# Kernel optimization log

Hardware: AMD Instinct MI355X
Metric: run time of the kernel (lower is better)

Reference implementation:

```python
import jax, jax.numpy as jnp
import numpy as np

B = 512      # batch
T = 16       # tokens per instruction
V = 1000     # vocab
E = 4        # num_experts
K = 1        # active experts per layer
NLAYERS = 3
TOPK_LOGIC = 32


def _conv(x, w, b, stride=2):
    # x: [B,Cin,H,W], w: [Cout,Cin,3,3] (OIHW), padding=1, stride=2
    y = jax.lax.conv_general_dilated(
        x, w, window_strides=(stride, stride), padding=((1, 1), (1, 1)),
        dimension_numbers=('NCHW', 'OIHW', 'NCHW'))
    return y + b[None, :, None, None]


def _gated_conv(x, w, b, gate):
    # w: [E,Cout,Cin,3,3], b: [E,Cout], gate: [B,E] 0/1 mask
    # Faithful to original: all experts computed densely, then masked.
    outs = jax.vmap(lambda wi, bi: _conv(x, wi, bi))(w, b)  # [E,B,Cout,H',W']
    return jnp.einsum('ebchw,be->bchw', outs, gate)


def _topk_mask(logits, k):
    # 0/1 mask with ones at the top-k positions along the last axis
    _, idx = jax.lax.top_k(logits, k)
    return jnp.sum(jax.nn.one_hot(idx, logits.shape[-1], dtype=logits.dtype), axis=-2)


def setup_inputs() -> dict:
    key = jax.random.key(0)
    ks = jax.random.split(key, 16)
    def rn(k, shape, s=0.05):
        return jax.random.normal(k, shape, jnp.float32) * s
    return dict(
        img=jax.random.normal(ks[0], (B, 12, 56, 56), jnp.float32),
        text=jax.random.randint(ks[1], (B, T), 0, V),
        prev_action=jax.random.randint(ks[2], (B,), 0, 7),
        emb_table=rn(ks[3], (V, 32), 1.0),
        r_w1=rn(ks[4], (32, 64)), r_b1=jnp.zeros((64,), jnp.float32),
        r_w2=rn(ks[5], (64, NLAYERS * E)), r_b2=jnp.zeros((NLAYERS * E,), jnp.float32),
        l_w1=rn(ks[6], (32, 64)), l_b1=jnp.zeros((64,), jnp.float32),
        l_w2=rn(ks[7], (64, 256)), l_b2=jnp.zeros((256,), jnp.float32),
        c1_w=rn(ks[8], (E, 32, 12, 3, 3)), c1_b=jnp.zeros((E, 32), jnp.float32),
        c2_w=rn(ks[9], (E, 64, 32, 3, 3)), c2_b=jnp.zeros((E, 64), jnp.float32),
        c3_w=rn(ks[10], (E, 128, 64, 3, 3)), c3_b=jnp.zeros((E, 128), jnp.float32),
        act_emb=rn(ks[11], (7, 16), 1.0),
        f_w=rn(ks[12], (6272 + 32 + 16, 256)), f_b=jnp.zeros((256,), jnp.float32),
        h_w=rn(ks[13], (256, 5)), h_b=jnp.zeros((5,), jnp.float32),
    )


def reference(img, text, prev_action, emb_table, r_w1, r_b1, r_w2, r_b2,
              l_w1, l_b1, l_w2, l_b2, c1_w, c1_b, c2_w, c2_b, c3_w, c3_b,
              act_emb, f_w, f_b, h_w, h_b):
    # EmbeddingBag(mode='mean') over token dim
    lang = jnp.mean(emb_table[text], axis=1)                      # [B,32]
    # Router: MLP -> [B,3,E] logits, top-k scatter -> 0/1 mask
    rlog = (jax.nn.relu(lang @ r_w1 + r_b1) @ r_w2 + r_b2).reshape(-1, NLAYERS, E)
    masks = _topk_mask(rlog, K)                                   # [B,3,E]
    x = jax.nn.relu(_gated_conv(img, c1_w, c1_b, masks[:, 0, :])) # [B,32,28,28]
    x = jax.nn.relu(_gated_conv(x, c2_w, c2_b, masks[:, 1, :]))   # [B,64,14,14]
    x = jax.nn.relu(_gated_conv(x, c3_w, c3_b, masks[:, 2, :]))   # [B,128,7,7]
    vis = x.reshape(x.shape[0], -1)                               # [B,6272]
    act = act_emb[prev_action]                                    # [B,16]
    fused = jnp.concatenate([vis, lang, act], axis=1)             # [B,6320]
    hidden = fused @ f_w + f_b                                    # [B,256]
    logic = jax.nn.relu(lang @ l_w1 + l_b1) @ l_w2 + l_b2         # [B,256]
    lmask = _topk_mask(logic, TOPK_LOGIC)                         # [B,256]
    out = jax.nn.relu(hidden * lmask)                             # dropout is identity in eval
    logits = out @ h_w + h_b                                      # [B,5]
    return logits, rlog
```

## Files before the change

kernel.cpp:

```cpp
#include <hip/hip_runtime.h>
#include <hip/hip_bf16.h>


typedef __bf16 bf16x8 __attribute__((ext_vector_type(8)));
typedef float f32x4 __attribute__((ext_vector_type(4)));
typedef unsigned short u16x8 __attribute__((ext_vector_type(8)));

__device__ __forceinline__ unsigned short f2bf(float f) {
  union { float f; unsigned u; } v; v.f = f;
  unsigned r = v.u + 0x7FFFu + ((v.u >> 16) & 1u);
  return (unsigned short)(r >> 16);
}

__global__ __launch_bounds__(256) void prep_kernel(
    const int* __restrict__ text, const float* __restrict__ emb,
    const float* __restrict__ r_w1, const float* __restrict__ r_b1,
    const float* __restrict__ r_w2, const float* __restrict__ r_b2,
    const float* __restrict__ l_w1, const float* __restrict__ l_b1,
    const float* __restrict__ l_w2, const float* __restrict__ l_b2,
    const float* __restrict__ act_emb, const int* __restrict__ pa,
    const float* __restrict__ c1_w, const float* __restrict__ c2_w,
    const float* __restrict__ c3_w, const float* __restrict__ fw,
    float* __restrict__ rlog_out, int* __restrict__ eidx, float* __restrict__ lmask,
    unsigned short* __restrict__ tailb,
    unsigned short* __restrict__ wb1, unsigned short* __restrict__ wb2,
    unsigned short* __restrict__ wb3, unsigned short* __restrict__ fwT) {
  __shared__ __align__(16) char shm[64 * 72 * 2];
  const int blk = blockIdx.x;
  const int tid = threadIdx.x;

  if (blk < 512) {
    int b = blk;
    int t = tid;
    __shared__ float lg[32];
    __shared__ float hr[64];
    __shared__ float hl[64];
    __shared__ float rl[12];
    __shared__ float lgc[256];

    if (t < 32) {
      const int* tb = text + b * 16;
      float s = 0.f;
#pragma unroll
      for (int tok = 0; tok < 16; ++tok) s += emb[tb[tok] * 32 + t];
      lg[t] = s * 0.0625f;
    }
    __syncthreads();

    if (t < 64) {
      float s1 = r_b1[t], s2 = l_b1[t];
      for (int k = 0; k < 32; ++k) {
        float lv = lg[k];
        s1 += lv * r_w1[k * 64 + t];
        s2 += lv * l_w1[k * 64 + t];
      }
      hr[t] = fmaxf(s1, 0.f);
      hl[t] = fmaxf(s2, 0.f);
    }
    if (t < 64) {
      float v = 0.f;
      if (t < 32) v = lg[t];
      else if (t < 48) v = act_emb[pa[b] * 16 + (t - 32)];
      tailb[b * 64 + t] = f2bf(v);
    }
    __syncthreads();

    if (t < 12) {
      float s = r_b2[t];
      for (int k = 0; k < 64; ++k) s += hr[k] * r_w2[k * 12 + t];
      rl[t] = s;
      rlog_out[b * 12 + t] = s;
    }
    {
      float s = l_b2[t];
      for (int k = 0; k < 64; ++k) s += hl[k] * l_w2[k * 256 + t];
      lgc[t] = s;
    }
    __syncthreads();

    if (t < 3) {
      int best = 0;
      float bv = rl[t * 4];
      for (int e = 1; e < 4; ++e) {
        float v = rl[t * 4 + e];
        if (v > bv) { bv = v; best = e; }
      }
      eidx[b * 3 + t] = best;
    }
    {
      float v = lgc[t];
      int cnt = 0;
      for (int k = 0; k < 256; ++k) {
        float u = lgc[k];
        cnt += (u > v) || (u == v && k < t);
      }
      lmask[b * 256 + t] = (cnt < 32) ? 1.f : 0.f;
    }
  } else if (blk < 2080) {
    int idx = (blk - 512) * 256 + tid;
    if (idx < 24576) {
      int k = idx % 192, ec = idx / 192;
      float v = 0.f;
      if (k < 144) {
        int g = k >> 4, ci = k & 15;
        if (ci < 12) v = c1_w[ec * 108 + ci * 9 + g];
      }
      wb1[idx] = f2bf(v);
    } else if (idx < 106496) {
      int i2 = idx - 24576;
      int k = i2 % 320, ec = i2 / 320;
      float v = 0.f;
      if (k < 288) {
        int g = k >> 5, ci = k & 31;
        v = c2_w[ec * 288 + ci * 9 + g];
      }
      wb2[i2] = f2bf(v);
    } else {
      int i3 = idx - 106496;
      int k = i3 % 576, ec = i3 / 576;
      int g = k >> 6, ci = k & 63;
      wb3[i3] = f2bf(c3_w[ec * 576 + ci * 9 + g]);
    }
  } else {
    unsigned short(*tl)[72] = (unsigned short(*)[72])shm;
    int fb = blk - 2080;
    int kblk = fb >> 2, nblk = fb & 3;
    int n0 = nblk * 64;
    int k0 = kblk * 64;
    int rl = tid >> 2;
    int c4 = (tid & 3) * 16;
    int srow;
    bool valid;
    if (kblk < 98) {
      int p = kblk >> 1;
      int c0 = (kblk & 1) * 64;
      srow = (c0 + rl) * 49 + p;
      valid = true;
    } else {
      srow = 6272 + rl;
      valid = (rl < 48);
    }
#pragma unroll
    for (int h = 0; h < 4; ++h) {
      float4 v = valid ? *(const float4*)&fw[(size_t)srow * 256 + n0 + c4 + h * 4]
                       : (float4){0.f, 0.f, 0.f, 0.f};
      tl[rl][c4 + h * 4 + 0] = f2bf(v.x);
      tl[rl][c4 + h * 4 + 1] = f2bf(v.y);
      tl[rl][c4 + h * 4 + 2] = f2bf(v.z);
      tl[rl][c4 + h * 4 + 3] = f2bf(v.w);
    }
    __syncthreads();
    int nloc = tid >> 2;
    int kc = (tid & 3) * 16;
    unsigned short vv[16];
#pragma unroll
    for (int i = 0; i < 16; ++i) vv[i] = tl[kc + i][nloc];
    unsigned short* dst = fwT + (size_t)(n0 + nloc) * 6336 + k0 + kc;
    *(uint4*)dst = *(const uint4*)&vv[0];
    *(uint4*)(dst + 8) = *(const uint4*)&vv[8];
  }
}

__global__ __launch_bounds__(256) void bucket_kernel(const int* __restrict__ eidx,
                                                     int* __restrict__ cnt,
                                                     int* __restrict__ perm) {
  int l = blockIdx.x;
  __shared__ int el[512];
  __shared__ int cc[4];
  int t = threadIdx.x;
  el[t] = eidx[t * 3 + l];
  el[t + 256] = eidx[(t + 256) * 3 + l];
  __syncthreads();
  if (t < 4) {
    int c = 0;
    for (int b = 0; b < 512; ++b) c += (el[b] == t);
    cc[t] = c;
    cnt[l * 4 + t] = c;
  }
  __syncthreads();
#pragma unroll
  for (int rep = 0; rep < 2; ++rep) {
    int b = t + rep * 256;
    int e = el[b];
    int rank = 0;
    for (int bp = 0; bp < b; ++bp) rank += (el[bp] == e);
    int off = 0;
    for (int ee = 0; ee < e; ++ee) off += cc[ee];
    perm[l * 512 + off + rank] = b;
  }
}

__global__ __launch_bounds__(256) void conv1_fused(
    const float* __restrict__ img, const unsigned short* __restrict__ wb,
    const float* __restrict__ bias, const int* __restrict__ eidx,
    unsigned short* __restrict__ out) {
  const int s = blockIdx.x / 7;
  const int t = blockIdx.x % 7;
  const int e = eidx[s * 3];
  __shared__ __align__(16) unsigned short lds_in[12288];
  __shared__ __align__(16) char ldsB[3 * 4096];
  const int tid = threadIdx.x;
  const int lane = tid & 63;
  const int wid = tid >> 6;
  const int wm0 = wid * 32;

  const int p0 = t * 128;
  const int ohmin = p0 / 28;
  const int ih0 = ohmin * 2 - 1;

  {
    uint4 z; z.x = z.y = z.z = z.w = 0u;
    uint4* q = (uint4*)lds_in;
#pragma unroll
    for (int i = 0; i < 6; ++i) q[tid + 256 * i] = z;
  }
  __syncthreads();

  for (int task = tid; task < 312; task += 256) {
    int row = task >> 1, half = task & 1;
    int ci = row / 13, ihl = row - ci * 13;
    int ih = ih0 + ihl;
    if ((unsigned)ih < 56u) {
      const float* src = img + (size_t)s * 37632 + ci * 3136 + ih * 56 + half * 28;
      unsigned short* dst = lds_in + ci * 728 + ihl * 56 + half * 28;
#pragma unroll
      for (int u = 0; u < 7; ++u) {
        float4 v = *(const float4*)(src + u * 4);
        unsigned short w4[4] = {f2bf(v.x), f2bf(v.y), f2bf(v.z), f2bf(v.w)};
        *(unsigned long long*)(dst + u * 4) = *(const unsigned long long*)w4;
      }
    }
  }
  {
    const unsigned short* wbe = wb + e * (32 * 192);
#pragma unroll
    for (int c = 0; c < 3; ++c) {
      int cc = tid + 256 * c;
      int n = cc / 24, cb = cc - n * 24;
      int kt = cb >> 3, cbl = cb & 7;
      uint4 v = *(const uint4*)(wbe + n * 192 + cb * 8);
      *(uint4*)(ldsB + kt * 4096 + n * 128 + ((cbl * 16) ^ ((n & 7) << 4))) = v;
    }
  }

  int ohr[2], owr[2];
#pragma unroll
  for (int mf = 0; mf < 2; ++mf) {
    int m = wm0 + mf * 16 + (lane & 15);
    int p = p0 + m;
    if (p > 783) p = 783;
    ohr[mf] = p / 28;
    owr[mf] = p - ohr[mf] * 28;
  }
  const int lg = lane >> 4;
  const int ci0 = (lg & 1) * 8;
  const int lgh = lg >> 1;
  int brdo[2], brx[2];
#pragma unroll
  for (int nf = 0; nf < 2; ++nf) {
    int n = nf * 16 + (lane & 15);
    brdo[nf] = n * 128;
    brx[nf] = (n & 7) << 4;
  }

  f32x4 acc[2][2];
#pragma unroll
  for (int mf = 0; mf < 2; ++mf)
#pragma unroll
    for (int nf = 0; nf < 2; ++nf) acc[mf][nf] = (f32x4){0.f, 0.f, 0.f, 0.f};

  __syncthreads();

#pragma unroll
  for (int kt = 0; kt < 3; ++kt) {
#pragma unroll
    for (int ks = 0; ks < 2; ++ks) {
      const int g = kt * 4 + ks * 2 + lgh;
      const int kh = g / 3;
      const int kw = g - kh * 3;
      bf16x8 af[2];
#pragma unroll
      for (int mf = 0; mf < 2; ++mf) {
        int iw = owr[mf] * 2 - 1 + kw;
        int ihl = (ohr[mf] - ohmin) * 2 + kh;
        bool valid = (g < 9) && (iw >= 0);
        const unsigned short* bp = lds_in + ci0 * 728 + ihl * 56 + iw;
        u16x8 a;
#pragma unroll
        for (int j = 0; j < 8; ++j) a[j] = valid ? bp[j * 728] : (unsigned short)0;
        af[mf] = __builtin_bit_cast(bf16x8, a);
      }
      bf16x8 bfv[2];
      const int cb = ks * 64 + ((lane >> 4) << 4);
#pragma unroll
      for (int nf = 0; nf < 2; ++nf)
        bfv[nf] = __builtin_bit_cast(bf16x8,
            *(const uint4*)(ldsB + kt * 4096 + brdo[nf] + (cb ^ brx[nf])));
#pragma unroll
      for (int mf = 0; mf < 2; ++mf)
#pragma unroll
        for (int nf = 0; nf < 2; ++nf)
          acc[mf][nf] = __builtin_amdgcn_mfma_f32_16x16x32_bf16(af[mf], bfv[nf], acc[mf][nf], 0, 0, 0);
    }
  }

  const int col = lane & 15;
  const int rg = (lane >> 4) * 4;
  const float b0 = bias[e * 32 + col];
  const float b1 = bias[e * 32 + 16 + col];
#pragma unroll
  for (int mf = 0; mf < 2; ++mf)
#pragma unroll
    for (int r = 0; r < 4; ++r) {
      int m = wm0 + mf * 16 + rg + r;
      int p = p0 + m;
      if (p < 784) {
        size_t ob = ((size_t)s * 784 + p) * 32;
        out[ob + col]      = f2bf(fmaxf(acc[mf][0][r] + b0, 0.f));
        out[ob + 16 + col] = f2bf(fmaxf(acc[mf][1][r] + b1, 0.f));
      }
    }
}

template<int CIN, int H, int OH, int KREAL, int KP, int COUT,
         int WGM, int WGN, int MF, int NF>
__global__ __launch_bounds__(256) void conv_mfma(
    const unsigned short* __restrict__ in, const unsigned short* __restrict__ wb,
    const float* __restrict__ bias, const int* __restrict__ cnt,
    const int* __restrict__ perm, unsigned short* __restrict__ out) {
  constexpr int PerS = OH * OH;
  constexpr int BM = WGM * MF * 16;
  constexpr int BN = WGN * NF * 16;
  constexpr int AJ = BM / 32;
  constexpr int KT = KP / 64;
  constexpr int W = H;
  constexpr int BCH = BN / 32;

  int bm = blockIdx.x;
  int e = 0, row0 = 0, rows = 0;
  bool found = false;
  {
    int acc = 0, ebase = 0;
#pragma unroll
    for (int ee = 0; ee < 4; ++ee) {
      int er = cnt[ee] * PerS;
      int te = (er + BM - 1) / BM;
      if (!found && bm < acc + te) {
        e = ee;
        row0 = ebase + (bm - acc) * BM;
        rows = er - (bm - acc) * BM;
        if (rows > BM) rows = BM;
        found = true;
      }
      acc += te;
      ebase += er;
    }
  }
  if (!found) return;

  __shared__ __align__(16) char lds[BM * 128 + BN * 128];
  char* ldsB = lds + BM * 128;
  const int tid = threadIdx.x;
  const int lane = tid & 63;
  const int wid = tid >> 6;
  const int wm0 = (wid / WGN) * (MF * 16);
  const int wn0 = (wid % WGN) * (NF * 16);
  const int c16 = tid & 7;

  int ihc[AJ], iwc[AJ], abase[AJ], adso[AJ];
#pragma unroll
  for (int j = 0; j < AJ; ++j) {
    int r = (tid >> 3) + 32 * j;
    int gr = row0 + r;
    const int MAXR = 512 * PerS - 1;
    if (gr > MAXR) gr = MAXR;
    int sord = gr / PerS;
    int p = gr - sord * PerS;
    int s = perm[sord];
    int oh = p / OH, ow = p - oh * OH;
    ihc[j] = oh * 2 - 1;
    iwc[j] = ow * 2 - 1;
    abase[j] = s * (H * W);
    adso[j] = r * 128 + ((c16 * 16) ^ ((r & 7) << 4));
  }
  const unsigned short* wbe = wb + (size_t)e * COUT * KP;
  int bgo[BCH], bdso[BCH];
#pragma unroll
  for (int c = 0; c < BCH; ++c) {
    int cc = tid + 256 * c;
    int n = cc >> 3, cb = cc & 7;
    bgo[c] = n * KP + cb * 8;
    bdso[c] = n * 128 + ((cb * 16) ^ ((n & 7) << 4));
  }
  int ardo[MF], arx[MF], brdo[NF], brx[NF];
#pragma unroll
  for (int mf = 0; mf < MF; ++mf) {
    int r = wm0 + mf * 16 + (lane & 15);
    ardo[mf] = r * 128;
    arx[mf] = (r & 7) << 4;
  }
#pragma unroll
  for (int nf = 0; nf < NF; ++nf) {
    int n = wn0 + nf * 16 + (lane & 15);
    brdo[nf] = n * 128;
    brx[nf] = (n & 7) << 4;
  }

  auto loadA = [&](int kt, int j) -> uint4 {
    uint4 z; z.x = z.y = z.z = z.w = 0u;
    int kbase = kt * 64 + c16 * 8;
    if (kbase >= KREAL) return z;
    int g = kbase / CIN;
    int ci0 = kbase - g * CIN;
    int kh = g / 3, kw = g - (g / 3) * 3;
    int ih = ihc[j] + kh, iw = iwc[j] + kw;
    if ((unsigned)ih >= (unsigned)H || (unsigned)iw >= (unsigned)W) return z;
    const unsigned short* p = in + ((size_t)(abase[j] + ih * W + iw) * CIN + ci0);
    return *(const uint4*)p;
  };

  uint4 rA[AJ], rB[BCH];
#pragma unroll
  for (int j = 0; j < AJ; ++j) rA[j] = loadA(0, j);
#pragma unroll
  for (int c = 0; c < BCH; ++c) rB[c] = *(const uint4*)(wbe + bgo[c]);

  f32x4 acc[MF][NF];
#pragma unroll
  for (int mf = 0; mf < MF; ++mf)
#pragma unroll
    for (int nf = 0; nf < NF; ++nf) acc[mf][nf] = (f32x4){0.f, 0.f, 0.f, 0.f};

  for (int kt = 0; kt < KT; ++kt) {
    __syncthreads();
#pragma unroll
    for (int j = 0; j < AJ; ++j) *(uint4*)(lds + adso[j]) = rA[j];
#pragma unroll
    for (int c = 0; c < BCH; ++c) *(uint4*)(ldsB + bdso[c]) = rB[c];
    __syncthreads();
    if (kt + 1 < KT) {
#pragma unroll
      for (int j = 0; j < AJ; ++j) rA[j] = loadA(kt + 1, j);
#pragma unroll
      for (int c = 0; c < BCH; ++c) rB[c] = *(const uint4*)(wbe + bgo[c] + (kt + 1) * 64);
    }
#pragma unroll
    for (int ks = 0; ks < 2; ++ks) {
      int cb = ks * 64 + ((lane >> 4) << 4);
      bf16x8 af[MF], bfv[NF];
#pragma unroll
      for (int mf = 0; mf < MF; ++mf)
        af[mf] = __builtin_bit_cast(bf16x8, *(const uint4*)(lds + ardo[mf] + (cb ^ arx[mf])));
#pragma unroll
      for (int nf = 0; nf < NF; ++nf)
        bfv[nf] = __builtin_bit_cast(bf16x8, *(const uint4*)(ldsB + brdo[nf] + (cb ^ brx[nf])));
#pragma unroll
      for (int mf = 0; mf < MF; ++mf)
#pragma unroll
        for (int nf = 0; nf < NF; ++nf)
          acc[mf][nf] = __builtin_amdgcn_mfma_f32_16x16x32_bf16(af[mf], bfv[nf], acc[mf][nf], 0, 0, 0);
    }
  }

  const int col = lane & 15;
  const int rg = (lane >> 4) * 4;
#pragma unroll
  for (int mf = 0; mf < MF; ++mf) {
#pragma unroll
    for (int r = 0; r < 4; ++r) {
      int m = wm0 + mf * 16 + rg + r;
      if (m < rows) {
        int gr = row0 + m;
        int sord = gr / PerS;
        int p = gr - sord * PerS;
        int s = perm[sord];
        size_t ob = ((size_t)s * PerS + p) * COUT;
#pragma unroll
        for (int nf = 0; nf < NF; ++nf) {
          int co = wn0 + nf * 16 + col;
          float v = acc[mf][nf][r] + bias[e * COUT + co];
          out[ob + co] = f2bf(fmaxf(v, 0.f));
        }
      }
    }
  }
}

__global__ __launch_bounds__(256) void fgemm_kernel(
    const unsigned short* __restrict__ x3, const unsigned short* __restrict__ tail,
    const unsigned short* __restrict__ fwT, float* __restrict__ partial) {
  constexpr int MF = 2, NF = 2;
  const int row0 = blockIdx.x * 64;
  const int nc0 = blockIdx.y * 64;
  const int kz = blockIdx.z * 704;
  __shared__ __align__(16) char lds[64 * 128 + 64 * 128];
  char* ldsB = lds + 64 * 128;
  const int tid = threadIdx.x;
  const int lane = tid & 63;
  const int wid = tid >> 6;
  const int wm0 = (wid >> 1) * 32;
  const int wn0 = (wid & 1) * 32;
  const int c16 = tid & 7;
  int arow[2], adso[2];
#pragma unroll
  for (int j = 0; j < 2; ++j) {
    int r = (tid >> 3) + 32 * j;
    arow[j] = row0 + r;
    adso[j] = r * 128 + ((c16 * 16) ^ ((r & 7) << 4));
  }
  int bgo[2], bdso[2];
#pragma unroll
  for (int c = 0; c < 2; ++c) {
    int cc = tid + 256 * c;
    int n = cc >> 3, cb = cc & 7;
    bgo[c] = (nc0 + n) * 6336 + kz + cb * 8;
    bdso[c] = n * 128 + ((cb * 16) ^ ((n & 7) << 4));
  }
  int ardo[MF], arx[MF], brdo[NF], brx[NF];
#pragma unroll
  for (int mf = 0; mf < MF; ++mf) {
    int r = wm0 + mf * 16 + (lane & 15);
    ardo[mf] = r * 128; arx[mf] = (r & 7) << 4;
  }
#pragma unroll
  for (int nf = 0; nf < NF; ++nf) {
    int n = wn0 + nf * 16 + (lane & 15);
    brdo[nf] = n * 128; brx[nf] = (n & 7) << 4;
  }
  auto loadA = [&](int kt, int j) -> uint4 {
    int k = kz + kt * 64 + c16 * 8;
    const unsigned short* p;
    if (k < 6272) p = x3 + (size_t)arow[j] * 6272 + k;
    else p = tail + arow[j] * 64 + (k - 6272);
    return *(const uint4*)p;
  };
  uint4 rA[2], rB[2];
#pragma unroll
  for (int j = 0; j < 2; ++j) rA[j] = loadA(0, j);
#pragma unroll
  for (int c = 0; c < 2; ++c) rB[c] = *(const uint4*)(fwT + bgo[c]);
  f32x4 acc[MF][NF];
#pragma unroll
  for (int mf = 0; mf < MF; ++mf)
#pragma unroll
    for (int nf = 0; nf < NF; ++nf) acc[mf][nf] = (f32x4){0.f, 0.f, 0.f, 0.f};

  for (int kt = 0; kt < 11; ++kt) {
    __syncthreads();
#pragma unroll
    for (int j = 0; j < 2; ++j) *(uint4*)(lds + adso[j]) = rA[j];
#pragma unroll
    for (int c = 0; c < 2; ++c) *(uint4*)(ldsB + bdso[c]) = rB[c];
    __syncthreads();
    if (kt + 1 < 11) {
#pragma unroll
      for (int j = 0; j < 2; ++j) rA[j] = loadA(kt + 1, j);
#pragma unroll
      for (int c = 0; c < 2; ++c) rB[c] = *(const uint4*)(fwT + bgo[c] + (kt + 1) * 64);
    }
#pragma unroll
    for (int ks = 0; ks < 2; ++ks) {
      int cb = ks * 64 + ((lane >> 4) << 4);
      bf16x8 af[MF], bfv[NF];
#pragma unroll
      for (int mf = 0; mf < MF; ++mf)
        af[mf] = __builtin_bit_cast(bf16x8, *(const uint4*)(lds + ardo[mf] + (cb ^ arx[mf])));
#pragma unroll
      for (int nf = 0; nf < NF; ++nf)
        bfv[nf] = __builtin_bit_cast(bf16x8, *(const uint4*)(ldsB + brdo[nf] + (cb ^ brx[nf])));
#pragma unroll
      for (int mf = 0; mf < MF; ++mf)
#pragma unroll
        for (int nf = 0; nf < NF; ++nf)
          acc[mf][nf] = __builtin_amdgcn_mfma_f32_16x16x32_bf16(af[mf], bfv[nf], acc[mf][nf], 0, 0, 0);
    }
  }
  const int col = lane & 15;
  const int rg = (lane >> 4) * 4;
  float* pz = partial + (size_t)blockIdx.z * 131072;
#pragma unroll
  for (int mf = 0; mf < MF; ++mf)
#pragma unroll
    for (int r = 0; r < 4; ++r) {
      int m = wm0 + mf * 16 + rg + r;
      int grow = row0 + m;
#pragma unroll
      for (int nf = 0; nf < NF; ++nf) {
        int n = nc0 + wn0 + nf * 16 + col;
        pz[grow * 256 + n] = acc[mf][nf][r];
      }
    }
}

__global__ __launch_bounds__(256) void reduce_head(const float* __restrict__ part,
                                                   const float* __restrict__ f_b,
                                                   const float* __restrict__ lmask,
                                                   const float* __restrict__ h_w,
                                                   const float* __restrict__ h_b,
                                                   float* __restrict__ logits) {
  int b = blockIdx.x, t = threadIdx.x;
  float s = f_b[t];
#pragma unroll
  for (int z = 0; z < 9; ++z) s += part[z * 131072 + b * 256 + t];
  __shared__ float o[256];
  o[t] = (lmask[b * 256 + t] != 0.f) ? fmaxf(s, 0.f) : 0.f;
  __syncthreads();
  if (t < 5) {
    float v = h_b[t];
    for (int n = 0; n < 256; ++n) v += o[n] * h_w[n * 5 + t];
    logits[b * 5 + t] = v;
  }
}

extern "C" void kernel_launch(void* const* d_in, const int* in_sizes, int n_in,
                              void* d_out, int out_size, void* d_ws, size_t ws_size,
                              hipStream_t stream) {
  (void)in_sizes; (void)n_in; (void)out_size; (void)ws_size;
  const float* img       = (const float*)d_in[0];
  const int*   text      = (const int*)d_in[1];
  const int*   pa        = (const int*)d_in[2];
  const float* emb_table = (const float*)d_in[3];
  const float* r_w1 = (const float*)d_in[4];
  const float* r_b1 = (const float*)d_in[5];
  const float* r_w2 = (const float*)d_in[6];
  const float* r_b2 = (const float*)d_in[7];
  const float* l_w1 = (const float*)d_in[8];
  const float* l_b1 = (const float*)d_in[9];
  const float* l_w2 = (const float*)d_in[10];
  const float* l_b2 = (const float*)d_in[11];
  const float* c1_w = (const float*)d_in[12];
  const float* c1_b = (const float*)d_in[13];
  const float* c2_w = (const float*)d_in[14];
  const float* c2_b = (const float*)d_in[15];
  const float* c3_w = (const float*)d_in[16];
  const float* c3_b = (const float*)d_in[17];
  const float* act_emb = (const float*)d_in[18];
  const float* f_w = (const float*)d_in[19];
  const float* f_b = (const float*)d_in[20];
  const float* h_w = (const float*)d_in[21];
  const float* h_b = (const float*)d_in[22];

  float* outf   = (float*)d_out;
  float* logits = outf;
  float* rlog   = outf + 2560;

  char* cur = (char*)d_ws;
  auto alloc = [&](size_t bytes) { char* r = cur; cur += (bytes + 255) & ~(size_t)255; return r; };
  float* lmask   = (float*)alloc(131072 * 4);
  int* eidx      = (int*)alloc(1536 * 4);
  int* cnt       = (int*)alloc(12 * 4);
  int* perm      = (int*)alloc(1536 * 4);
  unsigned short* wb1  = (unsigned short*)alloc((size_t)24576 * 2);
  unsigned short* wb2  = (unsigned short*)alloc((size_t)81920 * 2);
  unsigned short* wb3  = (unsigned short*)alloc((size_t)294912 * 2);
  unsigned short* fwT  = (unsigned short*)alloc((size_t)1622016 * 2);
  unsigned short* tailb= (unsigned short*)alloc((size_t)32768 * 2);
  unsigned short* x1b  = (unsigned short*)alloc((size_t)12845056 * 2);
  unsigned short* x2b  = (unsigned short*)alloc((size_t)6422528 * 2);
  unsigned short* x3b  = (unsigned short*)alloc((size_t)3211264 * 2);
  float* partial       = (float*)alloc((size_t)9 * 131072 * 4);

  prep_kernel<<<2476, 256, 0, stream>>>(text, emb_table,
                                        r_w1, r_b1, r_w2, r_b2,
                                        l_w1, l_b1, l_w2, l_b2,
                                        act_emb, pa,
                                        c1_w, c2_w, c3_w, f_w,
                                        rlog, eidx, lmask, tailb,
                                        wb1, wb2, wb3, fwT);
  bucket_kernel<<<3, 256, 0, stream>>>(eidx, cnt, perm);

  conv1_fused<<<3584, 256, 0, stream>>>(img, wb1, c1_b, eidx, x1b);
  conv_mfma<32, 28, 14, 288, 320, 64, 2, 2, 4, 2>
      <<<787, 256, 0, stream>>>(x1b, wb2, c2_b, cnt + 4, perm + 512, x2b);
  conv_mfma<64, 14, 7, 576, 576, 128, 1, 4, 4, 2>
      <<<395, 256, 0, stream>>>(x2b, wb3, c3_b, cnt + 8, perm + 1024, x3b);

  fgemm_kernel<<<dim3(8, 4, 9), 256, 0, stream>>>(x3b, tailb, fwT, partial);
  reduce_head<<<512, 256, 0, stream>>>(partial, f_b, lmask, h_w, h_b, logits);
}
```

Before: 151.2 us.

## Store conv1 input tile channel-innermost in LDS for vectorized A-fragment loads

The conv1 input tile in LDS changes from channel-major planes to a pixel-major layout with 16 channels innermost (32 bytes per pixel) and a left padding column. Each MFMA A fragment then comes from one 16-byte LDS read instead of eight scalar strided reads with per-element validity selects. An XOR swizzle spreads bank accesses, and invalid taps point at a zeroed padding row. The global-to-LDS fill now does scattered 2-byte stores, which may cost more, and the weight staging moves before the first barrier.

```diff
diff --git a/kernel.cpp b/kernel.cpp
--- a/kernel.cpp
+++ b/kernel.cpp
@@ -4,13 +4,14 @@
 
 typedef __bf16 bf16x8 __attribute__((ext_vector_type(8)));
 typedef float f32x4 __attribute__((ext_vector_type(4)));
-typedef unsigned short u16x8 __attribute__((ext_vector_type(8)));
 
 __device__ __forceinline__ unsigned short f2bf(float f) {
   union { float f; unsigned u; } v; v.f = f;
   unsigned r = v.u + 0x7FFFu + ((v.u >> 16) & 1u);
   return (unsigned short)(r >> 16);
 }
+
+__device__ __forceinline__ int wswz(int b) { return b ^ (((b >> 7) & 3) << 4); }
 
 __global__ __launch_bounds__(256) void prep_kernel(
     const int* __restrict__ text, const float* __restrict__ emb,
@@ -197,7 +198,7 @@
   const int s = blockIdx.x / 7;
   const int t = blockIdx.x % 7;
   const int e = eidx[s * 3];
-  __shared__ __align__(16) unsigned short lds_in[12288];
+  __shared__ __align__(16) char win[25536];
   __shared__ __align__(16) char ldsB[3 * 4096];
   const int tid = threadIdx.x;
   const int lane = tid & 63;
@@ -210,9 +211,18 @@
 
   {
     uint4 z; z.x = z.y = z.z = z.w = 0u;
-    uint4* q = (uint4*)lds_in;
-#pragma unroll
-    for (int i = 0; i < 6; ++i) q[tid + 256 * i] = z;
+    for (int i = tid; i < 1596; i += 256) ((uint4*)win)[i] = z;
+  }
+  {
+    const unsigned short* wbe = wb + e * (32 * 192);
+#pragma unroll
+    for (int c = 0; c < 3; ++c) {
+      int cc = tid + 256 * c;
+      int n = cc / 24, cb = cc - n * 24;
+      int kt = cb >> 3, cbl = cb & 7;
+      uint4 v = *(const uint4*)(wbe + n * 192 + cb * 8);
+      *(uint4*)(ldsB + kt * 4096 + n * 128 + ((cbl * 16) ^ ((n & 7) << 4))) = v;
+    }
   }
   __syncthreads();
 
@@ -222,35 +232,29 @@
     int ih = ih0 + ihl;
     if ((unsigned)ih < 56u) {
       const float* src = img + (size_t)s * 37632 + ci * 3136 + ih * 56 + half * 28;
-      unsigned short* dst = lds_in + ci * 728 + ihl * 56 + half * 28;
+      int base = (ihl * 57 + half * 28 + 1) * 32 + ci * 2;
 #pragma unroll
       for (int u = 0; u < 7; ++u) {
         float4 v = *(const float4*)(src + u * 4);
         unsigned short w4[4] = {f2bf(v.x), f2bf(v.y), f2bf(v.z), f2bf(v.w)};
-        *(unsigned long long*)(dst + u * 4) = *(const unsigned long long*)w4;
-      }
-    }
-  }
-  {
-    const unsigned short* wbe = wb + e * (32 * 192);
-#pragma unroll
-    for (int c = 0; c < 3; ++c) {
-      int cc = tid + 256 * c;
-      int n = cc / 24, cb = cc - n * 24;
-      int kt = cb >> 3, cbl = cb & 7;
-      uint4 v = *(const uint4*)(wbe + n * 192 + cb * 8);
-      *(uint4*)(ldsB + kt * 4096 + n * 128 + ((cbl * 16) ^ ((n & 7) << 4))) = v;
-    }
-  }
-
-  int ohr[2], owr[2];
+#pragma unroll
+        for (int q = 0; q < 4; ++q) {
+          int bp = base + (u * 4 + q) * 32;
+          *(unsigned short*)(win + wswz(bp)) = w4[q];
+        }
+      }
+    }
+  }
+
+  int ohl[2], owr[2];
 #pragma unroll
   for (int mf = 0; mf < 2; ++mf) {
     int m = wm0 + mf * 16 + (lane & 15);
     int p = p0 + m;
     if (p > 783) p = 783;
-    ohr[mf] = p / 28;
-    owr[mf] = p - ohr[mf] * 28;
+    int oh = p / 28;
+    owr[mf] = p - oh * 28;
+    ohl[mf] = (oh - ohmin) * 2;
   }
   const int lg = lane >> 4;
   const int ci0 = (lg & 1) * 8;
@@ -278,17 +282,15 @@
       const int g = kt * 4 + ks * 2 + lgh;
       const int kh = g / 3;
       const int kw = g - kh * 3;
+      const bool gv = (g < 9);
       bf16x8 af[2];
 #pragma unroll
       for (int mf = 0; mf < 2; ++mf) {
-        int iw = owr[mf] * 2 - 1 + kw;
-        int ihl = (ohr[mf] - ohmin) * 2 + kh;
-        bool valid = (g < 9) && (iw >= 0);
-        const unsigned short* bp = lds_in + ci0 * 728 + ihl * 56 + iw;
-        u16x8 a;
-#pragma unroll
-        for (int j = 0; j < 8; ++j) a[j] = valid ? bp[j * 728] : (unsigned short)0;
-        af[mf] = __builtin_bit_cast(bf16x8, a);
+        int iwp = owr[mf] * 2 + kw;
+        int ihl = ohl[mf] + kh;
+        int bp = gv ? ((ihl * 57 + iwp) * 32 + ci0 * 2)
+                    : (13 * 57 * 32 + ci0 * 2);
+        af[mf] = __builtin_bit_cast(bf16x8, *(const uint4*)(win + wswz(bp)));
       }
       bf16x8 bfv[2];
       const int cb = ks * 64 + ((lane >> 4) << 4);
```

New measurement: 148.0 us. 2.1% less time.
